# Optimization experiments

Hardware: AMD Instinct MI355X
Metric: run time of the kernel (lower is better)

## Reference

```python
import jax, jax.numpy as jnp
import numpy as np

N_NODES = 100_000
N_EDGES = 800_000
D_EDGE = 64
D_NODE = 64
D_GLOBAL = 64
D_IN = D_EDGE + 2 * D_NODE + D_GLOBAL  # 256
D_HID = 128
D_OUT = 64


def setup_inputs() -> dict:
    key = jax.random.key(0)
    ks = jax.random.split(key, 8)
    edge_feats = jax.random.normal(ks[0], (N_EDGES, D_EDGE), dtype=jnp.float32)
    node_feats = jax.random.normal(ks[1], (N_NODES, D_NODE), dtype=jnp.float32)
    global_attr = jax.random.normal(ks[2], (D_GLOBAL,), dtype=jnp.float32)
    senders = jax.random.randint(ks[3], (N_EDGES,), 0, N_NODES, dtype=jnp.int32)
    receivers = jax.random.randint(ks[4], (N_EDGES,), 0, N_NODES, dtype=jnp.int32)
    W1 = jax.random.normal(ks[5], (D_IN, D_HID), dtype=jnp.float32) * (1.0 / np.sqrt(D_IN))
    b1 = jnp.zeros((D_HID,), dtype=jnp.float32)
    W2 = jax.random.normal(ks[6], (D_HID, D_OUT), dtype=jnp.float32) * (1.0 / np.sqrt(D_HID))
    b2 = jnp.zeros((D_OUT,), dtype=jnp.float32)
    return {
        "edge_feats": edge_feats,
        "node_feats": node_feats,
        "global_attr": global_attr,
        "senders": senders,
        "receivers": receivers,
        "W1": W1, "b1": b1, "W2": W2, "b2": b2,
    }


def reference(edge_feats, node_feats, global_attr, senders, receivers, W1, b1, W2, b2):
    # Per-edge concat of [edge.data, receiver.data, sender.data, global.data]
    # (torch.cat order in the original), stacked over all edges.
    E = edge_feats.shape[0]
    recv = node_feats[receivers]          # [E, D_NODE] gather
    send = node_feats[senders]            # [E, D_NODE] gather
    g = jnp.broadcast_to(global_attr[None, :], (E, global_attr.shape[0]))
    x = jnp.concatenate([edge_feats, recv, send, g], axis=-1)  # [E, 256]
    # Updater MLP on the stacked edge batch.
    h = jax.nn.relu(x @ W1 + b1)          # [E, 128]
    out = h @ W2 + b2                     # [E, 64]
    return out
```

## Files before the change

### kernel.cpp

```cpp
#include <hip/hip_runtime.h>
#include <hip/hip_bf16.h>


typedef __bf16 bf16x8 __attribute__((ext_vector_type(8)));
typedef __bf16 bf16x2 __attribute__((ext_vector_type(2)));
typedef float f32x4 __attribute__((ext_vector_type(4)));

#define GRID_MAIN 1280
#define WS_NODEBF_OFF 66560

__global__ void prep_kernel(const float* __restrict__ W1, const float* __restrict__ b1,
                            const float* __restrict__ W2, const float* __restrict__ gattr,
                            __bf16* __restrict__ W1F, __bf16* __restrict__ W2F,
                            float* __restrict__ g1) {
    int tid = blockIdx.x * blockDim.x + threadIdx.x;
    if (tid < 128 * 192) {
        int n = tid / 192, k = tid % 192;
        int w = n >> 5, nt2 = (n >> 4) & 1, c = n & 15;
        int f = k >> 5, g = (k >> 3) & 3, j = k & 7;
        W1F[((((w * 2 + nt2) * 6 + f) * 64) + c + 16 * g) * 8 + j] = (__bf16)W1[k * 128 + n];
    } else if (tid < 128 * 192 + 64 * 128) {
        int t = tid - 128 * 192;
        int n = t / 128, p = t % 128;
        int w = n >> 4, c = n & 15;
        int ks = p >> 5, g = (p >> 3) & 3, j = p & 7;
        int klog = (p >> 5) * 32 + (p & 1) * 16 + ((p >> 1) & 15);
        W2F[(((w * 4 + ks) * 64) + c + 16 * g) * 8 + j] = (__bf16)W2[klog * 64 + n];
    } else if (tid < 128 * 192 + 64 * 128 + 128) {
        int n = tid - (128 * 192 + 64 * 128);
        float acc = b1[n];
        for (int j = 0; j < 64; ++j) acc += gattr[j] * W1[(192 + j) * 128 + n];
        g1[n] = acc;
    }
}

__global__ __launch_bounds__(256) void node_conv_kernel(const float* __restrict__ nf,
                                                        __bf16* __restrict__ nb, int n8) {
    int t = blockIdx.x * blockDim.x + threadIdx.x;
    if (t < n8) {
        f32x4 a = *(const f32x4*)(nf + (long)t * 8);
        f32x4 b = *(const f32x4*)(nf + (long)t * 8 + 4);
        bf16x8 o;
#pragma unroll
        for (int j = 0; j < 4; ++j) { o[j] = (__bf16)a[j]; o[4 + j] = (__bf16)b[j]; }
        *(bf16x8*)(nb + (long)t * 8) = o;
    }
}

__device__ __forceinline__ f32x4 mk4(float v) {
    f32x4 r; r[0] = v; r[1] = v; r[2] = v; r[3] = v; return r;
}

__device__ __forceinline__ bf16x8 cvt8(f32x4 lo, f32x4 hi) {
    bf16x8 t;
#pragma unroll
    for (int j = 0; j < 4; ++j) { t[j] = (__bf16)lo[j]; t[4 + j] = (__bf16)hi[j]; }
    return t;
}

__global__ __launch_bounds__(256) void edge_mlp_kernel(
    const float* __restrict__ edge_feats, const __bf16* __restrict__ node_bf,
    const int* __restrict__ senders, const int* __restrict__ receivers,
    const __bf16* __restrict__ W1F, const __bf16* __restrict__ W2F,
    const float* __restrict__ g1, const float* __restrict__ b2,
    float* __restrict__ out, int E, int numTiles)
{
    __shared__ __bf16 smem[4 * 6 * 64 * 8];

    const int lane = threadIdx.x & 63;
    const int w    = threadIdx.x >> 6;
    const int c    = lane & 15;
    const int g    = lane >> 4;
    const int G    = gridDim.x;

    bf16x8 wb1[2][6];
#pragma unroll
    for (int nt2 = 0; nt2 < 2; ++nt2)
#pragma unroll
        for (int f = 0; f < 6; ++f)
            wb1[nt2][f] = *(const bf16x8*)(W1F + (((w * 2 + nt2) * 6 + f) * 64 + lane) * 8);
    bf16x8 wb2[4];
#pragma unroll
    for (int ks = 0; ks < 4; ++ks)
        wb2[ks] = *(const bf16x8*)(W2F + ((w * 4 + ks) * 64 + lane) * 8);
    const float g1v0 = g1[w * 32 + c];
    const float g1v1 = g1[w * 32 + 16 + c];
    const float b2v  = b2[w * 16 + c];

    const int sr = (c * 4 + g) ^ (((c * 4 + g) >> 3) & 7);

    bf16x8 snr0, snr1, sns0, sns1;
    f32x4 se0, se1, se2, se3;
    int iR, iS;
    {
        long rc = (long)blockIdx.x * 64 + w * 16 + c;
        if (rc > (long)E - 1) rc = (long)E - 1;
        iR = receivers[rc]; iS = senders[rc];
        const __bf16* pr = node_bf + ((long)iR << 6) + g * 8;
        const __bf16* ps = node_bf + ((long)iS << 6) + g * 8;
        snr0 = *(const bf16x8*)(pr);
        snr1 = *(const bf16x8*)(pr + 32);
        sns0 = *(const bf16x8*)(ps);
        sns1 = *(const bf16x8*)(ps + 32);
        const float* pe = edge_feats + (rc << 6) + g * 8;
        se0 = *(const f32x4*)(pe);      se1 = *(const f32x4*)(pe + 4);
        se2 = *(const f32x4*)(pe + 32); se3 = *(const f32x4*)(pe + 36);
        if (blockIdx.x + G < numTiles) {
            long rc2 = (long)(blockIdx.x + G) * 64 + w * 16 + c;
            if (rc2 > (long)E - 1) rc2 = (long)E - 1;
            iR = receivers[rc2]; iS = senders[rc2];
        }
    }

    for (int t = blockIdx.x; t < numTiles; t += G) {
        __bf16* ab = smem + w * 6 * 512 + lane * 8;
        *(bf16x8*)(ab)        = cvt8(se0, se1);
        *(bf16x8*)(ab + 512)  = cvt8(se2, se3);
        *(bf16x8*)(ab + 1024) = snr0;
        *(bf16x8*)(ab + 1536) = snr1;
        *(bf16x8*)(ab + 2048) = sns0;
        *(bf16x8*)(ab + 2560) = sns1;

        const int tn = t + G;
        if (tn < numTiles) {
            const __bf16* pr = node_bf + ((long)iR << 6) + g * 8;
            const __bf16* ps = node_bf + ((long)iS << 6) + g * 8;
            snr0 = *(const bf16x8*)(pr);
            snr1 = *(const bf16x8*)(pr + 32);
            sns0 = *(const bf16x8*)(ps);
            sns1 = *(const bf16x8*)(ps + 32);
            long rce = (long)tn * 64 + w * 16 + c;
            if (rce > (long)E - 1) rce = (long)E - 1;
            const float* pe = edge_feats + (rce << 6) + g * 8;
            se0 = *(const f32x4*)(pe);      se1 = *(const f32x4*)(pe + 4);
            se2 = *(const f32x4*)(pe + 32); se3 = *(const f32x4*)(pe + 36);
            if (tn + G < numTiles) {
                long rc2 = (long)(tn + G) * 64 + w * 16 + c;
                if (rc2 > (long)E - 1) rc2 = (long)E - 1;
                iR = receivers[rc2]; iS = senders[rc2];
            }
        }
        __builtin_amdgcn_sched_barrier(0);

        asm volatile("s_waitcnt lgkmcnt(0)" ::: "memory");
        __builtin_amdgcn_s_barrier();

        f32x4 acc0[4], acc1[4];
#pragma unroll
        for (int mt = 0; mt < 4; ++mt) { acc0[mt] = mk4(g1v0); acc1[mt] = mk4(g1v1); }
#pragma unroll
        for (int mt = 0; mt < 4; ++mt)
#pragma unroll
            for (int f = 0; f < 6; ++f) {
                bf16x8 a = *(const bf16x8*)(smem + ((mt * 6 + f) * 64 + lane) * 8);
                acc0[mt] = __builtin_amdgcn_mfma_f32_16x16x32_bf16(a, wb1[0][f], acc0[mt], 0, 0, 0);
                acc1[mt] = __builtin_amdgcn_mfma_f32_16x16x32_bf16(a, wb1[1][f], acc1[mt], 0, 0, 0);
            }

        asm volatile("s_waitcnt lgkmcnt(0)" ::: "memory");
        __builtin_amdgcn_s_barrier();

#pragma unroll
        for (int mt = 0; mt < 4; ++mt)
#pragma unroll
            for (int r = 0; r < 4; ++r) {
                float v0 = acc0[mt][r]; v0 = v0 > 0.f ? v0 : 0.f;
                float v1 = acc1[mt][r]; v1 = v1 > 0.f ? v1 : 0.f;
                bf16x2 pk; pk[0] = (__bf16)v0; pk[1] = (__bf16)v1;
                int s = g * 16 + r * 4 + (c >> 2);
                s ^= (s >> 3) & 7;
                *(bf16x2*)&smem[(mt * 4 + w) * 512 + s * 8 + ((c & 3) << 1)] = pk;
            }

        asm volatile("s_waitcnt lgkmcnt(0)" ::: "memory");
        __builtin_amdgcn_s_barrier();

        f32x4 acc2[4];
#pragma unroll
        for (int mt = 0; mt < 4; ++mt) acc2[mt] = mk4(b2v);
#pragma unroll
        for (int mt = 0; mt < 4; ++mt)
#pragma unroll
            for (int ks = 0; ks < 4; ++ks) {
                bf16x8 ah = *(const bf16x8*)&smem[(mt * 4 + ks) * 512 + sr * 8];
                acc2[mt] = __builtin_amdgcn_mfma_f32_16x16x32_bf16(ah, wb2[ks], acc2[mt], 0, 0, 0);
            }

#pragma unroll
        for (int mt = 0; mt < 4; ++mt)
#pragma unroll
            for (int r = 0; r < 4; ++r) {
                long orow = (long)t * 64 + mt * 16 + g * 4 + r;
                if (orow < E) out[orow * 64 + w * 16 + c] = acc2[mt][r];
            }

        asm volatile("s_waitcnt lgkmcnt(0)" ::: "memory");
        __builtin_amdgcn_s_barrier();
    }
}

__global__ __launch_bounds__(256) void edge_mlp_fallback(
    const float* __restrict__ edge_feats, const float* __restrict__ node_feats,
    const int* __restrict__ senders, const int* __restrict__ receivers,
    const __bf16* __restrict__ W1F, const __bf16* __restrict__ W2F,
    const float* __restrict__ g1, const float* __restrict__ b2,
    float* __restrict__ out, int E, int numTiles)
{
    __shared__ __bf16 A_lds[4 * 6 * 64 * 8];
    __shared__ __bf16 h_frag[4 * 4 * 64 * 8];
    const int lane = threadIdx.x & 63;
    const int w = threadIdx.x >> 6;
    const int c = lane & 15;
    const int g = lane >> 4;
    const int G = gridDim.x;

    bf16x8 wb1[2][6];
#pragma unroll
    for (int nt2 = 0; nt2 < 2; ++nt2)
#pragma unroll
        for (int f = 0; f < 6; ++f)
            wb1[nt2][f] = *(const bf16x8*)(W1F + (((w * 2 + nt2) * 6 + f) * 64 + lane) * 8);
    bf16x8 wb2[4];
#pragma unroll
    for (int ks = 0; ks < 4; ++ks)
        wb2[ks] = *(const bf16x8*)(W2F + ((w * 4 + ks) * 64 + lane) * 8);
    const float g1v0 = g1[w * 32 + c];
    const float g1v1 = g1[w * 32 + 16 + c];
    const float b2v  = b2[w * 16 + c];

    for (int t = blockIdx.x; t < numTiles; t += G) {
        long rowc = (long)t * 64 + w * 16 + c;
        if (rowc > (long)E - 1) rowc = (long)E - 1;
        int iR = receivers[rowc], iS = senders[rowc];
        const float* pr = node_feats + ((long)iR << 6) + g * 8;
        const float* ps = node_feats + ((long)iS << 6) + g * 8;
        const float* pe = edge_feats + (rowc << 6) + g * 8;
        f32x4 e0a = *(const f32x4*)(pe),      e0b = *(const f32x4*)(pe + 4);
        f32x4 e1a = *(const f32x4*)(pe + 32), e1b = *(const f32x4*)(pe + 36);
        f32x4 r0a = *(const f32x4*)(pr),      r0b = *(const f32x4*)(pr + 4);
        f32x4 r1a = *(const f32x4*)(pr + 32), r1b = *(const f32x4*)(pr + 36);
        f32x4 s0a = *(const f32x4*)(ps),      s0b = *(const f32x4*)(ps + 4);
        f32x4 s1a = *(const f32x4*)(ps + 32), s1b = *(const f32x4*)(ps + 36);

        __bf16* ab = A_lds + w * 6 * 512 + lane * 8;
        *(bf16x8*)(ab)        = cvt8(e0a, e0b);
        *(bf16x8*)(ab + 512)  = cvt8(e1a, e1b);
        *(bf16x8*)(ab + 1024) = cvt8(r0a, r0b);
        *(bf16x8*)(ab + 1536) = cvt8(r1a, r1b);
        *(bf16x8*)(ab + 2048) = cvt8(s0a, s0b);
        *(bf16x8*)(ab + 2560) = cvt8(s1a, s1b);
        __syncthreads();

        f32x4 acc0[4], acc1[4];
#pragma unroll
        for (int mt = 0; mt < 4; ++mt) { acc0[mt] = mk4(g1v0); acc1[mt] = mk4(g1v1); }
#pragma unroll
        for (int mt = 0; mt < 4; ++mt)
#pragma unroll
            for (int f = 0; f < 6; ++f) {
                bf16x8 a = *(const bf16x8*)(A_lds + ((mt * 6 + f) * 64 + lane) * 8);
                acc0[mt] = __builtin_amdgcn_mfma_f32_16x16x32_bf16(a, wb1[0][f], acc0[mt], 0, 0, 0);
                acc1[mt] = __builtin_amdgcn_mfma_f32_16x16x32_bf16(a, wb1[1][f], acc1[mt], 0, 0, 0);
            }
#pragma unroll
        for (int mt = 0; mt < 4; ++mt)
#pragma unroll
            for (int r = 0; r < 4; ++r) {
                float v0 = acc0[mt][r]; v0 = v0 > 0.f ? v0 : 0.f;
                float v1 = acc1[mt][r]; v1 = v1 > 0.f ? v1 : 0.f;
                bf16x2 pk; pk[0] = (__bf16)v0; pk[1] = (__bf16)v1;
                *(bf16x2*)&h_frag[(((mt * 4 + w) * 64 + (g * 4 + r) * 4 + (c >> 2)) << 3)
                                  + ((c & 3) << 1)] = pk;
            }
        __syncthreads();

        f32x4 acc2[4];
#pragma unroll
        for (int mt = 0; mt < 4; ++mt) acc2[mt] = mk4(b2v);
#pragma unroll
        for (int mt = 0; mt < 4; ++mt)
#pragma unroll
            for (int ks = 0; ks < 4; ++ks) {
                bf16x8 ah = *(const bf16x8*)&h_frag[((mt * 4 + ks) * 64 + c * 4 + g) * 8];
                acc2[mt] = __builtin_amdgcn_mfma_f32_16x16x32_bf16(ah, wb2[ks], acc2[mt], 0, 0, 0);
            }
#pragma unroll
        for (int mt = 0; mt < 4; ++mt)
#pragma unroll
            for (int r = 0; r < 4; ++r) {
                long orow = (long)t * 64 + mt * 16 + g * 4 + r;
                if (orow < E) out[orow * 64 + w * 16 + c] = acc2[mt][r];
            }
        __syncthreads();
    }
}

extern "C" void kernel_launch(void* const* d_in, const int* in_sizes, int n_in,
                              void* d_out, int out_size, void* d_ws, size_t ws_size,
                              hipStream_t stream) {
    const float* edge_feats = (const float*)d_in[0];
    const float* node_feats = (const float*)d_in[1];
    const float* gattr      = (const float*)d_in[2];
    const int*   senders    = (const int*)d_in[3];
    const int*   receivers  = (const int*)d_in[4];
    const float* W1         = (const float*)d_in[5];
    const float* b1         = (const float*)d_in[6];
    const float* W2         = (const float*)d_in[7];
    const float* b2         = (const float*)d_in[8];
    float* out = (float*)d_out;

    const int E = in_sizes[3];
    const int N = in_sizes[1] / 64;

    char* ws = (char*)d_ws;
    __bf16* W1F = (__bf16*)ws;
    __bf16* W2F = (__bf16*)(ws + 49152);
    float*  g1  = (float*)(ws + 49152 + 16384);
    __bf16* nodeBF = (__bf16*)(ws + WS_NODEBF_OFF);

    const size_t ws_needed = (size_t)WS_NODEBF_OFF + (size_t)N * 64 * 2;
    const bool useNB = ws_size >= ws_needed;

    int prep_total = 128 * 192 + 64 * 128 + 128;
    prep_kernel<<<(prep_total + 255) / 256, 256, 0, stream>>>(W1, b1, W2, gattr, W1F, W2F, g1);

    const int numTiles = (E + 63) / 64;
    int grid = numTiles < GRID_MAIN ? numTiles : GRID_MAIN;
    if (useNB) {
        int n8 = N * 8;
        node_conv_kernel<<<(n8 + 255) / 256, 256, 0, stream>>>(node_feats, nodeBF, n8);
        edge_mlp_kernel<<<grid, 256, 0, stream>>>(edge_feats, nodeBF, senders, receivers,
                                                  W1F, W2F, g1, b2, out, E, numTiles);
    } else {
        edge_mlp_fallback<<<grid, 256, 0, stream>>>(edge_feats, node_feats, senders, receivers,
                                                    W1F, W2F, g1, b2, out, E, numTiles);
    }
}
```

Before: 138.0 us.

## Precompute per-node W1 projections and gather them instead of raw node features

Adds a pre-pass that multiplies every node's features by the receiver and sender slices of W1 and stores the results in bf16 (N x 256). The edge kernel then gathers the projected rows, adds them, and runs only the edge-feature part of the first GEMM, so per-edge first-layer MFMA work falls from 256 input columns to 64. The gathered row per node is larger (256 bf16 values versus 64), which raises random-access traffic. The pre-summed projections are also rounded to bf16, adding error. The change also removes the software prefetch from the old path and raises the grid size.

New measurement: 204.4 us. 48.1% more time.

```diff
diff --git a/kernel.cpp b/kernel.cpp
--- a/kernel.cpp
+++ b/kernel.cpp
@@ -6,8 +6,9 @@
 typedef __bf16 bf16x2 __attribute__((ext_vector_type(2)));
 typedef float f32x4 __attribute__((ext_vector_type(4)));
 
-#define GRID_MAIN 1280
-#define WS_NODEBF_OFF 66560
+#define GRID_MAIN 2048
+#define SWZ(x) ((x) ^ (((x) >> 3) & 7))
+#define WS_AUX_OFF 66560
 
 __global__ void prep_kernel(const float* __restrict__ W1, const float* __restrict__ b1,
                             const float* __restrict__ W2, const float* __restrict__ gattr,
@@ -58,6 +59,201 @@
     return t;
 }
 
+__global__ __launch_bounds__(256) void prep_p_kernel(
+    const float* __restrict__ node_feats, const __bf16* __restrict__ W1F,
+    __bf16* __restrict__ P_ws, int N)
+{
+    __shared__ __bf16 A_lds[4 * 2 * 64 * 8];
+    __shared__ __bf16 o_tile[64][264];
+
+    const int lane = threadIdx.x & 63;
+    const int v    = threadIdx.x >> 6;
+    const int c    = lane & 15;
+    const int g    = lane >> 4;
+
+    bf16x8 wp[4][2];
+#pragma unroll
+    for (int nt = 0; nt < 4; ++nt)
+#pragma unroll
+        for (int f = 0; f < 2; ++f) {
+            int w1  = (v & 1) * 2 + (nt >> 1);
+            int nt2 = nt & 1;
+            int fw  = 2 + (v >> 1) * 2 + f;
+            wp[nt][f] = *(const bf16x8*)(W1F + (((w1 * 2 + nt2) * 6 + fw) * 64 + lane) * 8);
+        }
+
+    const int n0 = blockIdx.x * 64;
+    {
+        int row = n0 + v * 16 + c; if (row > N - 1) row = N - 1;
+        const float* p = node_feats + (long)row * 64 + g * 8;
+        f32x4 s0 = *(const f32x4*)(p);
+        f32x4 s1 = *(const f32x4*)(p + 4);
+        f32x4 s2 = *(const f32x4*)(p + 32);
+        f32x4 s3 = *(const f32x4*)(p + 36);
+        __bf16* ab = A_lds + (v * 2) * 512 + lane * 8;
+        *(bf16x8*)(ab)       = cvt8(s0, s1);
+        *(bf16x8*)(ab + 512) = cvt8(s2, s3);
+    }
+    __syncthreads();
+
+    f32x4 acc[4][4];
+#pragma unroll
+    for (int mt = 0; mt < 4; ++mt)
+#pragma unroll
+        for (int nt = 0; nt < 4; ++nt) acc[mt][nt] = mk4(0.f);
+#pragma unroll
+    for (int mt = 0; mt < 4; ++mt)
+#pragma unroll
+        for (int f = 0; f < 2; ++f) {
+            bf16x8 a = *(const bf16x8*)(A_lds + ((mt * 2 + f) * 64 + lane) * 8);
+#pragma unroll
+            for (int nt = 0; nt < 4; ++nt)
+                acc[mt][nt] = __builtin_amdgcn_mfma_f32_16x16x32_bf16(a, wp[nt][f], acc[mt][nt], 0, 0, 0);
+        }
+
+#pragma unroll
+    for (int mt = 0; mt < 4; ++mt)
+#pragma unroll
+        for (int nt = 0; nt < 4; ++nt)
+#pragma unroll
+            for (int r = 0; r < 4; ++r) {
+                int row  = mt * 16 + g * 4 + r;
+                int slot = (v >> 1) * 128 + ((v & 1) * 2 + (nt >> 1)) * 32 + 2 * c + (nt & 1);
+                o_tile[row][slot] = (__bf16)acc[mt][nt][r];
+            }
+    __syncthreads();
+
+    {
+        int row = threadIdx.x >> 2, q = threadIdx.x & 3;
+        long nrow = (long)n0 + row;
+        if (nrow < N) {
+#pragma unroll
+            for (int k = 0; k < 8; ++k) {
+                bf16x8 vld = *(const bf16x8*)&o_tile[row][q * 64 + k * 8];
+                *(bf16x8*)(P_ws + nrow * 256 + q * 64 + k * 8) = vld;
+            }
+        }
+    }
+}
+
+__global__ __launch_bounds__(256) void edge_mlp_p(
+    const float* __restrict__ edge_feats, const __bf16* __restrict__ P_ws,
+    const int* __restrict__ senders, const int* __restrict__ receivers,
+    const __bf16* __restrict__ W1F, const __bf16* __restrict__ W2F,
+    const float* __restrict__ g1, const float* __restrict__ b2,
+    float* __restrict__ out, int E, int numTiles)
+{
+    __shared__ __bf16 P_l[64 * 136];
+    __shared__ __bf16 h_frag[4 * 4 * 64 * 8];
+    char* pb = (char*)P_l;
+
+    const int lane = threadIdx.x & 63;
+    const int w    = threadIdx.x >> 6;
+    const int c    = lane & 15;
+    const int g    = lane >> 4;
+    const int G    = gridDim.x;
+
+    bf16x8 wb1[2][2];
+#pragma unroll
+    for (int nt2 = 0; nt2 < 2; ++nt2)
+#pragma unroll
+        for (int f = 0; f < 2; ++f)
+            wb1[nt2][f] = *(const bf16x8*)(W1F + (((w * 2 + nt2) * 6 + f) * 64 + lane) * 8);
+    bf16x8 wb2[4];
+#pragma unroll
+    for (int ks = 0; ks < 4; ++ks)
+        wb2[ks] = *(const bf16x8*)(W2F + ((w * 4 + ks) * 64 + lane) * 8);
+    const float g1v0 = g1[w * 32 + c];
+    const float g1v1 = g1[w * 32 + 16 + c];
+    const float b2v  = b2[w * 16 + c];
+    const int sr = SWZ(c * 4 + g);
+    const int eg = (lane >> 4);
+    const int ch = (lane & 15);
+
+    for (int t = blockIdx.x; t < numTiles; t += G) {
+        bf16x8 pr0, pr1, pr2, pr3, ps0, ps1, ps2, ps3;
+        {
+            long e0 = (long)t * 64 + w * 16 + eg;
+#pragma unroll
+            for (int j = 0; j < 4; ++j) {
+                long e = e0 + 4 * j; if (e > (long)E - 1) e = (long)E - 1;
+                int ir = receivers[e];
+                int is = senders[e];
+                bf16x8 a = *(const bf16x8*)(P_ws + (long)ir * 256 + ch * 8);
+                bf16x8 b = *(const bf16x8*)(P_ws + (long)is * 256 + 128 + ch * 8);
+                if (j == 0) { pr0 = a; ps0 = b; }
+                else if (j == 1) { pr1 = a; ps1 = b; }
+                else if (j == 2) { pr2 = a; ps2 = b; }
+                else { pr3 = a; ps3 = b; }
+            }
+        }
+#pragma unroll
+        for (int j = 0; j < 4; ++j) {
+            bf16x8 a = (j == 0) ? pr0 : (j == 1) ? pr1 : (j == 2) ? pr2 : pr3;
+            bf16x8 b = (j == 0) ? ps0 : (j == 1) ? ps1 : (j == 2) ? ps2 : ps3;
+            bf16x8 sm;
+#pragma unroll
+            for (int k = 0; k < 8; ++k) sm[k] = (__bf16)((float)a[k] + (float)b[k]);
+            *(bf16x8*)(pb + (w * 16 + 4 * j + eg) * 272 + ch * 16) = sm;
+        }
+
+        asm volatile("s_waitcnt lgkmcnt(0)" ::: "memory");
+        __builtin_amdgcn_s_barrier();
+
+        f32x4 acc0[4], acc1[4];
+#pragma unroll
+        for (int mt = 0; mt < 4; ++mt) { acc0[mt] = mk4(g1v0); acc1[mt] = mk4(g1v1); }
+#pragma unroll
+        for (int mt = 0; mt < 4; ++mt) {
+            long row = (long)t * 64 + mt * 16 + c; if (row > (long)E - 1) row = (long)E - 1;
+            const float* pe = edge_feats + row * 64 + g * 8;
+#pragma unroll
+            for (int f = 0; f < 2; ++f) {
+                bf16x8 a = cvt8(*(const f32x4*)(pe + f * 32), *(const f32x4*)(pe + f * 32 + 4));
+                acc0[mt] = __builtin_amdgcn_mfma_f32_16x16x32_bf16(a, wb1[0][f], acc0[mt], 0, 0, 0);
+                acc1[mt] = __builtin_amdgcn_mfma_f32_16x16x32_bf16(a, wb1[1][f], acc1[mt], 0, 0, 0);
+            }
+        }
+
+#pragma unroll
+        for (int mt = 0; mt < 4; ++mt)
+#pragma unroll
+            for (int r = 0; r < 4; ++r) {
+                int e = mt * 16 + g * 4 + r;
+                unsigned pu = *(const unsigned*)(pb + e * 272 + w * 64 + (c << 2));
+                float plo = __uint_as_float(pu << 16);
+                float phi = __uint_as_float(pu & 0xffff0000u);
+                float v0 = acc0[mt][r] + plo; v0 = v0 > 0.f ? v0 : 0.f;
+                float v1 = acc1[mt][r] + phi; v1 = v1 > 0.f ? v1 : 0.f;
+                bf16x2 pk; pk[0] = (__bf16)v0; pk[1] = (__bf16)v1;
+                int s = SWZ(g * 16 + r * 4 + (c >> 2));
+                *(bf16x2*)&h_frag[(mt * 4 + w) * 512 + s * 8 + ((c & 3) << 1)] = pk;
+            }
+
+        asm volatile("s_waitcnt lgkmcnt(0)" ::: "memory");
+        __builtin_amdgcn_s_barrier();
+
+        f32x4 acc2[4];
+#pragma unroll
+        for (int mt = 0; mt < 4; ++mt) acc2[mt] = mk4(b2v);
+#pragma unroll
+        for (int mt = 0; mt < 4; ++mt)
+#pragma unroll
+            for (int ks = 0; ks < 4; ++ks) {
+                bf16x8 ah = *(const bf16x8*)&h_frag[(mt * 4 + ks) * 512 + sr * 8];
+                acc2[mt] = __builtin_amdgcn_mfma_f32_16x16x32_bf16(ah, wb2[ks], acc2[mt], 0, 0, 0);
+            }
+
+#pragma unroll
+        for (int mt = 0; mt < 4; ++mt)
+#pragma unroll
+            for (int r = 0; r < 4; ++r) {
+                long orow = (long)t * 64 + mt * 16 + g * 4 + r;
+                if (orow < E) out[orow * 64 + w * 16 + c] = acc2[mt][r];
+            }
+    }
+}
+
 __global__ __launch_bounds__(256) void edge_mlp_kernel(
     const float* __restrict__ edge_feats, const __bf16* __restrict__ node_bf,
     const int* __restrict__ senders, const int* __restrict__ receivers,
@@ -65,7 +261,7 @@
     const float* __restrict__ g1, const float* __restrict__ b2,
     float* __restrict__ out, int E, int numTiles)
 {
-    __shared__ __bf16 smem[4 * 6 * 64 * 8];
+    __shared__ __bf16 smem[20480];
 
     const int lane = threadIdx.x & 63;
     const int w    = threadIdx.x >> 6;
@@ -86,62 +282,29 @@
     const float g1v0 = g1[w * 32 + c];
     const float g1v1 = g1[w * 32 + 16 + c];
     const float b2v  = b2[w * 16 + c];
-
-    const int sr = (c * 4 + g) ^ (((c * 4 + g) >> 3) & 7);
-
-    bf16x8 snr0, snr1, sns0, sns1;
-    f32x4 se0, se1, se2, se3;
-    int iR, iS;
-    {
-        long rc = (long)blockIdx.x * 64 + w * 16 + c;
+    const int sr = SWZ(c * 4 + g);
+
+    for (int t = blockIdx.x; t < numTiles; t += G) {
+        long rc = (long)t * 64 + w * 16 + c;
         if (rc > (long)E - 1) rc = (long)E - 1;
-        iR = receivers[rc]; iS = senders[rc];
+        int iR = receivers[rc], iS = senders[rc];
         const __bf16* pr = node_bf + ((long)iR << 6) + g * 8;
         const __bf16* ps = node_bf + ((long)iS << 6) + g * 8;
-        snr0 = *(const bf16x8*)(pr);
-        snr1 = *(const bf16x8*)(pr + 32);
-        sns0 = *(const bf16x8*)(ps);
-        sns1 = *(const bf16x8*)(ps + 32);
+        bf16x8 snr0 = *(const bf16x8*)(pr);
+        bf16x8 snr1 = *(const bf16x8*)(pr + 32);
+        bf16x8 sns0 = *(const bf16x8*)(ps);
+        bf16x8 sns1 = *(const bf16x8*)(ps + 32);
         const float* pe = edge_feats + (rc << 6) + g * 8;
-        se0 = *(const f32x4*)(pe);      se1 = *(const f32x4*)(pe + 4);
-        se2 = *(const f32x4*)(pe + 32); se3 = *(const f32x4*)(pe + 36);
-        if (blockIdx.x + G < numTiles) {
-            long rc2 = (long)(blockIdx.x + G) * 64 + w * 16 + c;
-            if (rc2 > (long)E - 1) rc2 = (long)E - 1;
-            iR = receivers[rc2]; iS = senders[rc2];
-        }
-    }
-
-    for (int t = blockIdx.x; t < numTiles; t += G) {
-        __bf16* ab = smem + w * 6 * 512 + lane * 8;
+        f32x4 se0 = *(const f32x4*)(pe);      f32x4 se1 = *(const f32x4*)(pe + 4);
+        f32x4 se2 = *(const f32x4*)(pe + 32); f32x4 se3 = *(const f32x4*)(pe + 36);
+
+        __bf16* ab = smem + w * 3072 + lane * 8;
         *(bf16x8*)(ab)        = cvt8(se0, se1);
         *(bf16x8*)(ab + 512)  = cvt8(se2, se3);
         *(bf16x8*)(ab + 1024) = snr0;
         *(bf16x8*)(ab + 1536) = snr1;
         *(bf16x8*)(ab + 2048) = sns0;
         *(bf16x8*)(ab + 2560) = sns1;
-
-        const int tn = t + G;
-        if (tn < numTiles) {
-            const __bf16* pr = node_bf + ((long)iR << 6) + g * 8;
-            const __bf16* ps = node_bf + ((long)iS << 6) + g * 8;
-            snr0 = *(const bf16x8*)(pr);
-            snr1 = *(const bf16x8*)(pr + 32);
-            sns0 = *(const bf16x8*)(ps);
-            sns1 = *(const bf16x8*)(ps + 32);
-            long rce = (long)tn * 64 + w * 16 + c;
-            if (rce > (long)E - 1) rce = (long)E - 1;
-            const float* pe = edge_feats + (rce << 6) + g * 8;
-            se0 = *(const f32x4*)(pe);      se1 = *(const f32x4*)(pe + 4);
-            se2 = *(const f32x4*)(pe + 32); se3 = *(const f32x4*)(pe + 36);
-            if (tn + G < numTiles) {
-                long rc2 = (long)(tn + G) * 64 + w * 16 + c;
-                if (rc2 > (long)E - 1) rc2 = (long)E - 1;
-                iR = receivers[rc2]; iS = senders[rc2];
-            }
-        }
-        __builtin_amdgcn_sched_barrier(0);
-
         asm volatile("s_waitcnt lgkmcnt(0)" ::: "memory");
         __builtin_amdgcn_s_barrier();
 
@@ -156,10 +319,6 @@
                 acc0[mt] = __builtin_amdgcn_mfma_f32_16x16x32_bf16(a, wb1[0][f], acc0[mt], 0, 0, 0);
                 acc1[mt] = __builtin_amdgcn_mfma_f32_16x16x32_bf16(a, wb1[1][f], acc1[mt], 0, 0, 0);
             }
-
-        asm volatile("s_waitcnt lgkmcnt(0)" ::: "memory");
-        __builtin_amdgcn_s_barrier();
-
 #pragma unroll
         for (int mt = 0; mt < 4; ++mt)
 #pragma unroll
@@ -167,11 +326,9 @@
                 float v0 = acc0[mt][r]; v0 = v0 > 0.f ? v0 : 0.f;
                 float v1 = acc1[mt][r]; v1 = v1 > 0.f ? v1 : 0.f;
                 bf16x2 pk; pk[0] = (__bf16)v0; pk[1] = (__bf16)v1;
-                int s = g * 16 + r * 4 + (c >> 2);
-                s ^= (s >> 3) & 7;
-                *(bf16x2*)&smem[(mt * 4 + w) * 512 + s * 8 + ((c & 3) << 1)] = pk;
-            }
-
+                int s = SWZ(g * 16 + r * 4 + (c >> 2));
+                *(bf16x2*)&smem[12288 + (mt * 4 + w) * 512 + s * 8 + ((c & 3) << 1)] = pk;
+            }
         asm volatile("s_waitcnt lgkmcnt(0)" ::: "memory");
         __builtin_amdgcn_s_barrier();
 
@@ -182,10 +339,9 @@
         for (int mt = 0; mt < 4; ++mt)
 #pragma unroll
             for (int ks = 0; ks < 4; ++ks) {
-                bf16x8 ah = *(const bf16x8*)&smem[(mt * 4 + ks) * 512 + sr * 8];
+                bf16x8 ah = *(const bf16x8*)&smem[12288 + (mt * 4 + ks) * 512 + sr * 8];
                 acc2[mt] = __builtin_amdgcn_mfma_f32_16x16x32_bf16(ah, wb2[ks], acc2[mt], 0, 0, 0);
             }
-
 #pragma unroll
         for (int mt = 0; mt < 4; ++mt)
 #pragma unroll
@@ -193,105 +349,8 @@
                 long orow = (long)t * 64 + mt * 16 + g * 4 + r;
                 if (orow < E) out[orow * 64 + w * 16 + c] = acc2[mt][r];
             }
-
-        asm volatile("s_waitcnt lgkmcnt(0)" ::: "memory");
-        __builtin_amdgcn_s_barrier();
-    }
-}
-
-__global__ __launch_bounds__(256) void edge_mlp_fallback(
-    const float* __restrict__ edge_feats, const float* __restrict__ node_feats,
-    const int* __restrict__ senders, const int* __restrict__ receivers,
-    const __bf16* __restrict__ W1F, const __bf16* __restrict__ W2F,
-    const float* __restrict__ g1, const float* __restrict__ b2,
-    float* __restrict__ out, int E, int numTiles)
-{
-    __shared__ __bf16 A_lds[4 * 6 * 64 * 8];
-    __shared__ __bf16 h_frag[4 * 4 * 64 * 8];
-    const int lane = threadIdx.x & 63;
-    const int w = threadIdx.x >> 6;
-    const int c = lane & 15;
-    const int g = lane >> 4;
-    const int G = gridDim.x;
-
-    bf16x8 wb1[2][6];
-#pragma unroll
-    for (int nt2 = 0; nt2 < 2; ++nt2)
-#pragma unroll
-        for (int f = 0; f < 6; ++f)
-            wb1[nt2][f] = *(const bf16x8*)(W1F + (((w * 2 + nt2) * 6 + f) * 64 + lane) * 8);
-    bf16x8 wb2[4];
-#pragma unroll
-    for (int ks = 0; ks < 4; ++ks)
-        wb2[ks] = *(const bf16x8*)(W2F + ((w * 4 + ks) * 64 + lane) * 8);
-    const float g1v0 = g1[w * 32 + c];
-    const float g1v1 = g1[w * 32 + 16 + c];
-    const float b2v  = b2[w * 16 + c];
-
-    for (int t = blockIdx.x; t < numTiles; t += G) {
-        long rowc = (long)t * 64 + w * 16 + c;
-        if (rowc > (long)E - 1) rowc = (long)E - 1;
-        int iR = receivers[rowc], iS = senders[rowc];
-        const float* pr = node_feats + ((long)iR << 6) + g * 8;
-        const float* ps = node_feats + ((long)iS << 6) + g * 8;
-        const float* pe = edge_feats + (rowc << 6) + g * 8;
-        f32x4 e0a = *(const f32x4*)(pe),      e0b = *(const f32x4*)(pe + 4);
-        f32x4 e1a = *(const f32x4*)(pe + 32), e1b = *(const f32x4*)(pe + 36);
-        f32x4 r0a = *(const f32x4*)(pr),      r0b = *(const f32x4*)(pr + 4);
-        f32x4 r1a = *(const f32x4*)(pr + 32), r1b = *(const f32x4*)(pr + 36);
-        f32x4 s0a = *(const f32x4*)(ps),      s0b = *(const f32x4*)(ps + 4);
-        f32x4 s1a = *(const f32x4*)(ps + 32), s1b = *(const f32x4*)(ps + 36);
-
-        __bf16* ab = A_lds + w * 6 * 512 + lane * 8;
-        *(bf16x8*)(ab)        = cvt8(e0a, e0b);
-        *(bf16x8*)(ab + 512)  = cvt8(e1a, e1b);
-        *(bf16x8*)(ab + 1024) = cvt8(r0a, r0b);
-        *(bf16x8*)(ab + 1536) = cvt8(r1a, r1b);
-        *(bf16x8*)(ab + 2048) = cvt8(s0a, s0b);
-        *(bf16x8*)(ab + 2560) = cvt8(s1a, s1b);
-        __syncthreads();
-
-        f32x4 acc0[4], acc1[4];
-#pragma unroll
-        for (int mt = 0; mt < 4; ++mt) { acc0[mt] = mk4(g1v0); acc1[mt] = mk4(g1v1); }
-#pragma unroll
-        for (int mt = 0; mt < 4; ++mt)
-#pragma unroll
-            for (int f = 0; f < 6; ++f) {
-                bf16x8 a = *(const bf16x8*)(A_lds + ((mt * 6 + f) * 64 + lane) * 8);
-                acc0[mt] = __builtin_amdgcn_mfma_f32_16x16x32_bf16(a, wb1[0][f], acc0[mt], 0, 0, 0);
-                acc1[mt] = __builtin_amdgcn_mfma_f32_16x16x32_bf16(a, wb1[1][f], acc1[mt], 0, 0, 0);
-            }
-#pragma unroll
-        for (int mt = 0; mt < 4; ++mt)
-#pragma unroll
-            for (int r = 0; r < 4; ++r) {
-                float v0 = acc0[mt][r]; v0 = v0 > 0.f ? v0 : 0.f;
-                float v1 = acc1[mt][r]; v1 = v1 > 0.f ? v1 : 0.f;
-                bf16x2 pk; pk[0] = (__bf16)v0; pk[1] = (__bf16)v1;
-                *(bf16x2*)&h_frag[(((mt * 4 + w) * 64 + (g * 4 + r) * 4 + (c >> 2)) << 3)
-                                  + ((c & 3) << 1)] = pk;
-            }
-        __syncthreads();
-
-        f32x4 acc2[4];
-#pragma unroll
-        for (int mt = 0; mt < 4; ++mt) acc2[mt] = mk4(b2v);
-#pragma unroll
-        for (int mt = 0; mt < 4; ++mt)
-#pragma unroll
-            for (int ks = 0; ks < 4; ++ks) {
-                bf16x8 ah = *(const bf16x8*)&h_frag[((mt * 4 + ks) * 64 + c * 4 + g) * 8];
-                acc2[mt] = __builtin_amdgcn_mfma_f32_16x16x32_bf16(ah, wb2[ks], acc2[mt], 0, 0, 0);
-            }
-#pragma unroll
-        for (int mt = 0; mt < 4; ++mt)
-#pragma unroll
-            for (int r = 0; r < 4; ++r) {
-                long orow = (long)t * 64 + mt * 16 + g * 4 + r;
-                if (orow < E) out[orow * 64 + w * 16 + c] = acc2[mt][r];
-            }
-        __syncthreads();
+        asm volatile("s_waitcnt lgkmcnt(0)" ::: "memory");
+        __builtin_amdgcn_s_barrier();
     }
 }
 
@@ -316,23 +375,23 @@
     __bf16* W1F = (__bf16*)ws;
     __bf16* W2F = (__bf16*)(ws + 49152);
     float*  g1  = (float*)(ws + 49152 + 16384);
-    __bf16* nodeBF = (__bf16*)(ws + WS_NODEBF_OFF);
-
-    const size_t ws_needed = (size_t)WS_NODEBF_OFF + (size_t)N * 64 * 2;
-    const bool useNB = ws_size >= ws_needed;
+    __bf16* aux = (__bf16*)(ws + WS_AUX_OFF);
 
     int prep_total = 128 * 192 + 64 * 128 + 128;
     prep_kernel<<<(prep_total + 255) / 256, 256, 0, stream>>>(W1, b1, W2, gattr, W1F, W2F, g1);
 
     const int numTiles = (E + 63) / 64;
     int grid = numTiles < GRID_MAIN ? numTiles : GRID_MAIN;
-    if (useNB) {
+
+    const size_t ws_need_P = (size_t)WS_AUX_OFF + (size_t)N * 256 * 2;
+    if (ws_size >= ws_need_P) {
+        prep_p_kernel<<<(N + 63) / 64, 256, 0, stream>>>(node_feats, W1F, aux, N);
+        edge_mlp_p<<<grid, 256, 0, stream>>>(edge_feats, aux, senders, receivers,
+                                             W1F, W2F, g1, b2, out, E, numTiles);
+    } else {
         int n8 = N * 8;
-        node_conv_kernel<<<(n8 + 255) / 256, 256, 0, stream>>>(node_feats, nodeBF, n8);
-        edge_mlp_kernel<<<grid, 256, 0, stream>>>(edge_feats, nodeBF, senders, receivers,
+        node_conv_kernel<<<(n8 + 255) / 256, 256, 0, stream>>>(node_feats, aux, n8);
+        edge_mlp_kernel<<<grid, 256, 0, stream>>>(edge_feats, aux, senders, receivers,
                                                   W1F, W2F, g1, b2, out, E, numTiles);
-    } else {
-        edge_mlp_fallback<<<grid, 256, 0, stream>>>(edge_feats, node_feats, senders, receivers,
-                                                    W1F, W2F, g1, b2, out, E, numTiles);
-    }
-}
+    }
+}
```
